# Kernel tuning notes

Hardware: AMD Instinct MI355X
Metric: run time of the kernel (lower is better)

Reference implementation:

```python
import jax, jax.numpy as jnp
import numpy as np

# ---- module hyperparams (match init_kwargs) ----
IN_CH, OUT_CH = 32, 64
KERNEL = 9
STRIDE, PADDING = 1, 4
GRID_SIZE, SPLINE_ORDER = 5, 3
GRID_LO, GRID_HI = -1.0, 1.0
NUM_COEF = GRID_SIZE + SPLINE_ORDER  # 8 spline basis functions


def make_grid():
    h = (GRID_HI - GRID_LO) / GRID_SIZE
    # extended knot vector, same for every input feature (efficient-KAN)
    return (jnp.arange(-SPLINE_ORDER, GRID_SIZE + SPLINE_ORDER + 1, dtype=jnp.float32) * h + GRID_LO)


def b_splines(x, grid, order):
    """Cox-de Boor B-spline bases. x: (...,) -> (..., NUM_COEF)."""
    x = x[..., None]
    bases = ((x >= grid[:-1]) & (x < grid[1:])).astype(x.dtype)
    for k in range(1, order + 1):
        left = (x - grid[: -(k + 1)]) / (grid[k:-1] - grid[: -(k + 1)])
        right = (grid[k + 1:] - x) / (grid[k + 1:] - grid[1:-k])
        bases = left * bases[..., :-1] + right * bases[..., 1:]
    return bases


def setup_inputs() -> dict:
    key = jax.random.key(0)
    k1, k2, k3, k4 = jax.random.split(key, 4)
    x = jax.random.normal(k1, (16, IN_CH, 2048), dtype=jnp.float32)
    # all O*I KANLinear(kernel->1) modules batched into single tensors
    base_w = jax.random.normal(k2, (OUT_CH, IN_CH, KERNEL), dtype=jnp.float32) * (1.0 / np.sqrt(KERNEL))
    spline_w = jax.random.normal(k3, (OUT_CH, IN_CH, KERNEL, NUM_COEF), dtype=jnp.float32) * 0.1
    spline_scaler = jax.random.normal(k4, (OUT_CH, IN_CH, KERNEL), dtype=jnp.float32) * (1.0 / np.sqrt(KERNEL))
    return {"x": x, "base_w": base_w, "spline_w": spline_w, "spline_scaler": spline_scaler}


def reference(x, base_w, spline_w, spline_scaler):
    grid = make_grid()
    B, I, L = x.shape
    L_out = (L + 2 * PADDING - (KERNEL - 1) - 1) // STRIDE + 1  # dilation=1
    xp = jnp.pad(x, ((0, 0), (0, 0), (PADDING, PADDING)))
    # sliding windows: (B, I, L_out, K)
    idx = jnp.arange(L_out)[:, None] * STRIDE + jnp.arange(KERNEL)[None, :]
    win = xp[:, :, idx]
    # base branch: silu(window) . base_weight, summed over in_channels
    out = jnp.einsum('bilk,oik->bol', jax.nn.silu(win), base_w)
    # spline branch
    bs = b_splines(win, grid, SPLINE_ORDER)          # (B, I, L_out, K, C)
    sw = spline_w * spline_scaler[..., None]         # scaled spline weight
    out = out + jnp.einsum('bilkc,oikc->bol', bs, sw)
    return out
```

## Files before the change

kernel.cpp:

```cpp
#include <hip/hip_runtime.h>
#include <hip/hip_bf16.h>

namespace {

constexpr int KIN  = 32;
constexpr int KOUT = 64;
constexpr int KW   = 9;
constexpr int KPAD = 4;
constexpr int LIN  = 2048;
constexpr int KTOT = 2592;

typedef __bf16 bf16x8 __attribute__((ext_vector_type(8)));
typedef float  f32x4  __attribute__((ext_vector_type(4)));
typedef unsigned short u16x4 __attribute__((ext_vector_type(4)));
typedef unsigned short u16x8 __attribute__((ext_vector_type(8)));

__device__ __forceinline__ unsigned short f2bf(float x) {
    unsigned int u = __float_as_uint(x);
    u += 0x7FFFu + ((u >> 16) & 1u);
    return (unsigned short)(u >> 16);
}

__device__ __forceinline__ float bf2f(unsigned short h) {
    return __uint_as_float((unsigned int)h << 16);
}

#define MFMA16(a, b, c) __builtin_amdgcn_mfma_f32_16x16x32_bf16((a), (b), (c), 0, 0, 0)

__global__ __launch_bounds__(256) void kan_wprep(const float* __restrict__ base_w,
                                                 const float* __restrict__ spline_w,
                                                 const float* __restrict__ spline_scaler,
                                                 unsigned short* __restrict__ Wf) {
    unsigned int idx = blockIdx.x * 256 + threadIdx.x;
    unsigned int ch  = idx >> 8;
    unsigned int m   = (idx >> 6) & 3;
    unsigned int lane = idx & 63;
    unsigned int o  = m * 16 + (lane & 15);
    unsigned int kb = ch * 32 + (lane >> 4) * 8;

    u16x8 pk;
#pragma unroll
    for (int e = 0; e < 8; ++e) {
        unsigned int kappa = kb + e;
        unsigned int k  = kappa / 288;
        unsigned int r2 = kappa - k * 288;
        unsigned int i  = r2 / 9;
        unsigned int c  = r2 - i * 9;
        unsigned int t  = o * 288 + i * 9 + k;
        float val = (c == 0) ? base_w[t]
                             : spline_w[(size_t)t * 8 + (c - 1)] * spline_scaler[t];
        pk[e] = f2bf(val);
    }
    *(u16x8*)(Wf + (size_t)idx * 8) = pk;
}

constexpr int BN     = 64;
constexpr int TROW   = 72;
constexpr int F2COLS = 296;

__global__ __launch_bounds__(512, 4) void kan_fused(const float* __restrict__ x,
                                                    const unsigned short* __restrict__ Wf,
                                                    float* __restrict__ out) {
    __shared__ __align__(16) char smem[65536];
    unsigned short* f2t = (unsigned short*)smem;

    int tid  = threadIdx.x;
    int lane = tid & 63;
    int wv   = tid >> 6;
    int lo = lane & 15, hi = lane >> 4;

    int blk = blockIdx.x;
    int b   = blk >> 5;
    int l0  = (blk & 31) * BN;

    const int ch0 = 10 * wv;
    constexpr int NCHW = 10;
    int kk = ch0 / 9;
    int jb = ch0 - kk * 9;
    const unsigned short* wp = Wf + (size_t)ch0 * 2048 + (size_t)lane * 8;
    bf16x8 a0 = *(const bf16x8*)(wp);
    bf16x8 a1 = *(const bf16x8*)(wp + 512);
    bf16x8 a2 = *(const bf16x8*)(wp + 1024);
    bf16x8 a3 = *(const bf16x8*)(wp + 1536);

    float vv[5];
#pragma unroll
    for (int p = 0; p < 5; ++p) {
        int unit = p * 512 + tid;
        bool ok = unit < TROW * KIN;
        int i = unit / TROW;
        int r = unit - i * TROW;
        int gx = l0 + r - KPAD;
        vv[p] = 0.f;
        if (ok && gx >= 0 && gx < LIN) vv[p] = x[((size_t)b * KIN + i) * LIN + gx];
    }

    {
        f32x4 z = (f32x4){0.f, 0.f, 0.f, 0.f};
        for (int c = tid; c < TROW * F2COLS / 8; c += 512)
            *(f32x4*)(f2t + (size_t)c * 8) = z;
    }
    __syncthreads();

#pragma unroll
    for (int p = 0; p < 5; ++p) {
        int unit = p * 512 + tid;
        bool ok = unit < TROW * KIN;
        int i = unit / TROW;
        int r = unit - i * TROW;
        float v = vv[p];
        if (ok) {
            unsigned short* row = f2t + (size_t)r * F2COLS + i * 9;
            row[0] = f2bf(v / (1.f + __expf(-v)));
            float t5 = (v + 2.2f) * 2.5f;
            float mf = floorf(t5);
            int   m  = (int)mf;
            float u  = t5 - mf;
            float u2 = u * u, u3 = u2 * u;
            float w  = 1.f - u;
            float P0 = u3 * (1.f / 6.f);
            float P3 = w * w * w * (1.f / 6.f);
            float P1 = (1.f / 6.f) + 0.5f * u + 0.5f * u2 - 0.5f * u3;
            float P2 = (4.f / 6.f) - u2 + 0.5f * u3;
            int c0 = m - 3;
            if ((unsigned)(c0 + 0) <= 7u) row[1 + c0 + 0] = f2bf(P3);
            if ((unsigned)(c0 + 1) <= 7u) row[1 + c0 + 1] = f2bf(P2);
            if ((unsigned)(c0 + 2) <= 7u) row[1 + c0 + 2] = f2bf(P1);
            if ((unsigned)(c0 + 3) <= 7u) row[1 + c0 + 3] = f2bf(P0);
        }
    }
    __syncthreads();

    f32x4 acc[4][4];
#pragma unroll
    for (int m = 0; m < 4; ++m)
#pragma unroll
        for (int n = 0; n < 4; ++n) acc[m][n] = (f32x4){0.f, 0.f, 0.f, 0.f};

    const unsigned short* fp = f2t + (size_t)(lo + kk) * F2COLS + jb * 32 + hi * 8;
    bf16x8 b0 = *(const bf16x8*)(fp);
    bf16x8 b1 = *(const bf16x8*)(fp + 16 * F2COLS);
    bf16x8 b2 = *(const bf16x8*)(fp + 32 * F2COLS);
    bf16x8 b3 = *(const bf16x8*)(fp + 48 * F2COLS);

    for (int t = 0; t < NCHW; ++t) {
        bool last = (t + 1 == NCHW);
        const unsigned short* wpn = last ? wp : wp + 2048;
        int jb2 = last ? jb : jb + 1;
        const unsigned short* fpn = last ? fp : fp + ((jb2 == 9) ? (F2COLS - 8 * 32) : 32);
        if (jb2 == 9) jb2 = 0;

        bf16x8 na0 = *(const bf16x8*)(wpn);
        bf16x8 na1 = *(const bf16x8*)(wpn + 512);
        bf16x8 na2 = *(const bf16x8*)(wpn + 1024);
        bf16x8 na3 = *(const bf16x8*)(wpn + 1536);

        __builtin_amdgcn_s_setprio(1);
        acc[0][0] = MFMA16(a0, b0, acc[0][0]);
        acc[1][0] = MFMA16(a1, b0, acc[1][0]);
        acc[2][0] = MFMA16(a2, b0, acc[2][0]);
        acc[3][0] = MFMA16(a3, b0, acc[3][0]);
        b0 = *(const bf16x8*)(fpn);
        acc[0][1] = MFMA16(a0, b1, acc[0][1]);
        acc[1][1] = MFMA16(a1, b1, acc[1][1]);
        acc[2][1] = MFMA16(a2, b1, acc[2][1]);
        acc[3][1] = MFMA16(a3, b1, acc[3][1]);
        b1 = *(const bf16x8*)(fpn + 16 * F2COLS);
        acc[0][2] = MFMA16(a0, b2, acc[0][2]);
        acc[1][2] = MFMA16(a1, b2, acc[1][2]);
        acc[2][2] = MFMA16(a2, b2, acc[2][2]);
        acc[3][2] = MFMA16(a3, b2, acc[3][2]);
        b2 = *(const bf16x8*)(fpn + 32 * F2COLS);
        acc[0][3] = MFMA16(a0, b3, acc[0][3]);
        acc[1][3] = MFMA16(a1, b3, acc[1][3]);
        acc[2][3] = MFMA16(a2, b3, acc[2][3]);
        acc[3][3] = MFMA16(a3, b3, acc[3][3]);
        b3 = *(const bf16x8*)(fpn + 48 * F2COLS);
        __builtin_amdgcn_s_setprio(0);

        a0 = na0; a1 = na1; a2 = na2; a3 = na3;
        wp = wpn; fp = fpn; jb = jb2;
    }

    {
        int mq = wv & 3;
        int np = wv >> 2;
        bf16x8 a80 = *(const bf16x8*)(Wf + (size_t)80 * 2048 + (size_t)mq * 512 + (size_t)lane * 8);
        const unsigned short* fp80 = f2t + (size_t)(lo + 8) * F2COLS + 8 * 32 + hi * 8;
        bf16x8 bA = *(const bf16x8*)(fp80 + (size_t)(2 * np) * 16 * F2COLS);
        bf16x8 bB = *(const bf16x8*)(fp80 + (size_t)(2 * np + 1) * 16 * F2COLS);
        switch (wv) {
        case 0: acc[0][0] = MFMA16(a80, bA, acc[0][0]); acc[0][1] = MFMA16(a80, bB, acc[0][1]); break;
        case 1: acc[1][0] = MFMA16(a80, bA, acc[1][0]); acc[1][1] = MFMA16(a80, bB, acc[1][1]); break;
        case 2: acc[2][0] = MFMA16(a80, bA, acc[2][0]); acc[2][1] = MFMA16(a80, bB, acc[2][1]); break;
        case 3: acc[3][0] = MFMA16(a80, bA, acc[3][0]); acc[3][1] = MFMA16(a80, bB, acc[3][1]); break;
        case 4: acc[0][2] = MFMA16(a80, bA, acc[0][2]); acc[0][3] = MFMA16(a80, bB, acc[0][3]); break;
        case 5: acc[1][2] = MFMA16(a80, bA, acc[1][2]); acc[1][3] = MFMA16(a80, bB, acc[1][3]); break;
        case 6: acc[2][2] = MFMA16(a80, bA, acc[2][2]); acc[2][3] = MFMA16(a80, bB, acc[2][3]); break;
        case 7: acc[3][2] = MFMA16(a80, bA, acc[3][2]); acc[3][3] = MFMA16(a80, bB, acc[3][3]); break;
        }
    }

    __syncthreads();
    unsigned short* red16 = (unsigned short*)smem;
#pragma unroll
    for (int m = 0; m < 4; ++m)
#pragma unroll
        for (int n = 0; n < 4; ++n) {
            int sid = m * 4 + n;
            f32x4 a = acc[m][n];
            u16x4 pk = (u16x4){f2bf(a[0]), f2bf(a[1]), f2bf(a[2]), f2bf(a[3])};
            *(u16x4*)(red16 + (((size_t)sid * 8 + wv) * 64 + lane) * 4) = pk;
        }
    __syncthreads();
#pragma unroll
    for (int s = 0; s < 2; ++s) {
        int sid = wv * 2 + s;
        int m = sid >> 2, n = sid & 3;
        f32x4 acc_s = (f32x4){0.f, 0.f, 0.f, 0.f};
#pragma unroll
        for (int w = 0; w < 8; ++w) {
            u16x4 pk = *(const u16x4*)(red16 + (((size_t)sid * 8 + w) * 64 + lane) * 4);
            acc_s[0] += bf2f(pk[0]);
            acc_s[1] += bf2f(pk[1]);
            acc_s[2] += bf2f(pk[2]);
            acc_s[3] += bf2f(pk[3]);
        }
        int o = m * 16 + hi * 4;
        float* op = out + ((size_t)b * KOUT + o) * LIN + l0 + n * 16 + lo;
        op[0]               = acc_s[0];
        op[LIN]             = acc_s[1];
        op[2 * LIN]         = acc_s[2];
        op[3 * (size_t)LIN] = acc_s[3];
    }
}

}

extern "C" void kernel_launch(void* const* d_in, const int* in_sizes, int n_in,
                              void* d_out, int out_size, void* d_ws, size_t ws_size,
                              hipStream_t stream) {
    const float* x             = (const float*)d_in[0];
    const float* base_w        = (const float*)d_in[1];
    const float* spline_w      = (const float*)d_in[2];
    const float* spline_scaler = (const float*)d_in[3];
    float* out = (float*)d_out;

    unsigned short* Wf = (unsigned short*)d_ws;

    kan_wprep<<<81, 256, 0, stream>>>(base_w, spline_w, spline_scaler, Wf);
    kan_fused<<<512, 512, 0, stream>>>(x, Wf, out);
}
```

Measured before the change: 22.86 us.

## Halve block to 4 waves with 20 K-chunks each and shrink shared memory

The fused kernel now launches 256 threads (4 waves) per block instead of 512, and each wave covers 20 K-chunks instead of 10. The tail chunk and the split-K reduction are reworked for four partial sums instead of eight. Shared memory is cut from 64KB to the exact feature tile size, so more blocks can sit on a CU. This trades less cross-wave reduction traffic and better occupancy per block for a longer serial MFMA chain per wave and more loads per thread during feature generation.

```diff
diff --git a/kernel.cpp b/kernel.cpp
--- a/kernel.cpp
+++ b/kernel.cpp
@@ -58,10 +58,10 @@
 constexpr int TROW   = 72;
 constexpr int F2COLS = 296;
 
-__global__ __launch_bounds__(512, 4) void kan_fused(const float* __restrict__ x,
+__global__ __launch_bounds__(256, 3) void kan_fused(const float* __restrict__ x,
                                                     const unsigned short* __restrict__ Wf,
                                                     float* __restrict__ out) {
-    __shared__ __align__(16) char smem[65536];
+    __shared__ __align__(16) char smem[TROW * F2COLS * 2];
     unsigned short* f2t = (unsigned short*)smem;
 
     int tid  = threadIdx.x;
@@ -73,8 +73,8 @@
     int b   = blk >> 5;
     int l0  = (blk & 31) * BN;
 
-    const int ch0 = 10 * wv;
-    constexpr int NCHW = 10;
+    const int ch0 = 20 * wv;
+    constexpr int NCHW = 20;
     int kk = ch0 / 9;
     int jb = ch0 - kk * 9;
     const unsigned short* wp = Wf + (size_t)ch0 * 2048 + (size_t)lane * 8;
@@ -83,51 +83,47 @@
     bf16x8 a2 = *(const bf16x8*)(wp + 1024);
     bf16x8 a3 = *(const bf16x8*)(wp + 1536);
 
-    float vv[5];
-#pragma unroll
-    for (int p = 0; p < 5; ++p) {
-        int unit = p * 512 + tid;
-        bool ok = unit < TROW * KIN;
+    float vv[9];
+#pragma unroll
+    for (int p = 0; p < 9; ++p) {
+        int unit = p * 256 + tid;
         int i = unit / TROW;
         int r = unit - i * TROW;
         int gx = l0 + r - KPAD;
         vv[p] = 0.f;
-        if (ok && gx >= 0 && gx < LIN) vv[p] = x[((size_t)b * KIN + i) * LIN + gx];
+        if (gx >= 0 && gx < LIN) vv[p] = x[((size_t)b * KIN + i) * LIN + gx];
     }
 
     {
         f32x4 z = (f32x4){0.f, 0.f, 0.f, 0.f};
-        for (int c = tid; c < TROW * F2COLS / 8; c += 512)
+        for (int c = tid; c < TROW * F2COLS / 8; c += 256)
             *(f32x4*)(f2t + (size_t)c * 8) = z;
     }
     __syncthreads();
 
 #pragma unroll
-    for (int p = 0; p < 5; ++p) {
-        int unit = p * 512 + tid;
-        bool ok = unit < TROW * KIN;
+    for (int p = 0; p < 9; ++p) {
+        int unit = p * 256 + tid;
         int i = unit / TROW;
         int r = unit - i * TROW;
         float v = vv[p];
-        if (ok) {
-            unsigned short* row = f2t + (size_t)r * F2COLS + i * 9;
-            row[0] = f2bf(v / (1.f + __expf(-v)));
-            float t5 = (v + 2.2f) * 2.5f;
-            float mf = floorf(t5);
-            int   m  = (int)mf;
-            float u  = t5 - mf;
-            float u2 = u * u, u3 = u2 * u;
-            float w  = 1.f - u;
-            float P0 = u3 * (1.f / 6.f);
-            float P3 = w * w * w * (1.f / 6.f);
-            float P1 = (1.f / 6.f) + 0.5f * u + 0.5f * u2 - 0.5f * u3;
-            float P2 = (4.f / 6.f) - u2 + 0.5f * u3;
-            int c0 = m - 3;
-            if ((unsigned)(c0 + 0) <= 7u) row[1 + c0 + 0] = f2bf(P3);
-            if ((unsigned)(c0 + 1) <= 7u) row[1 + c0 + 1] = f2bf(P2);
-            if ((unsigned)(c0 + 2) <= 7u) row[1 + c0 + 2] = f2bf(P1);
-            if ((unsigned)(c0 + 3) <= 7u) row[1 + c0 + 3] = f2bf(P0);
-        }
+        unsigned short* row = f2t + (size_t)r * F2COLS + i * 9;
+        row[0] = f2bf(v / (1.f + __expf(-v)));
+        float t5 = (v + 2.2f) * 2.5f;
+        float mf = floorf(t5);
+        int   m  = (int)mf;
+        float u  = t5 - mf;
+        float u2 = u * u, u3 = u2 * u;
+        float w  = 1.f - u;
+        float P0 = u3 * (1.f / 6.f);
+        float P3 = w * w * w * (1.f / 6.f);
+        float P1 = (1.f / 6.f) + 0.5f * u + 0.5f * u2 - 0.5f * u3;
+        float P2 = (4.f / 6.f) - u2 + 0.5f * u3;
+        int c0 = m - 3;
+        if ((unsigned)(c0 + 0) <= 7u) row[1 + c0 + 0] = f2bf(P3);
+        if ((unsigned)(c0 + 1) <= 7u) row[1 + c0 + 1] = f2bf(P2);
+        if ((unsigned)(c0 + 2) <= 7u) row[1 + c0 + 2] = f2bf(P1);
+        if ((unsigned)(c0 + 3) <= 7u) row[1 + c0 + 3] = f2bf(P0);
     }
     __syncthreads();
 
@@ -183,21 +179,21 @@
     }
 
     {
-        int mq = wv & 3;
-        int np = wv >> 2;
-        bf16x8 a80 = *(const bf16x8*)(Wf + (size_t)80 * 2048 + (size_t)mq * 512 + (size_t)lane * 8);
+        bf16x8 a80 = *(const bf16x8*)(Wf + (size_t)80 * 2048 + (size_t)wv * 512 + (size_t)lane * 8);
         const unsigned short* fp80 = f2t + (size_t)(lo + 8) * F2COLS + 8 * 32 + hi * 8;
-        bf16x8 bA = *(const bf16x8*)(fp80 + (size_t)(2 * np) * 16 * F2COLS);
-        bf16x8 bB = *(const bf16x8*)(fp80 + (size_t)(2 * np + 1) * 16 * F2COLS);
+        bf16x8 bA = *(const bf16x8*)(fp80);
+        bf16x8 bB = *(const bf16x8*)(fp80 + 16 * F2COLS);
+        bf16x8 bC = *(const bf16x8*)(fp80 + 32 * F2COLS);
+        bf16x8 bD = *(const bf16x8*)(fp80 + 48 * F2COLS);
         switch (wv) {
-        case 0: acc[0][0] = MFMA16(a80, bA, acc[0][0]); acc[0][1] = MFMA16(a80, bB, acc[0][1]); break;
-        case 1: acc[1][0] = MFMA16(a80, bA, acc[1][0]); acc[1][1] = MFMA16(a80, bB, acc[1][1]); break;
-        case 2: acc[2][0] = MFMA16(a80, bA, acc[2][0]); acc[2][1] = MFMA16(a80, bB, acc[2][1]); break;
-        case 3: acc[3][0] = MFMA16(a80, bA, acc[3][0]); acc[3][1] = MFMA16(a80, bB, acc[3][1]); break;
-        case 4: acc[0][2] = MFMA16(a80, bA, acc[0][2]); acc[0][3] = MFMA16(a80, bB, acc[0][3]); break;
-        case 5: acc[1][2] = MFMA16(a80, bA, acc[1][2]); acc[1][3] = MFMA16(a80, bB, acc[1][3]); break;
-        case 6: acc[2][2] = MFMA16(a80, bA, acc[2][2]); acc[2][3] = MFMA16(a80, bB, acc[2][3]); break;
-        case 7: acc[3][2] = MFMA16(a80, bA, acc[3][2]); acc[3][3] = MFMA16(a80, bB, acc[3][3]); break;
+        case 0: acc[0][0]=MFMA16(a80,bA,acc[0][0]); acc[0][1]=MFMA16(a80,bB,acc[0][1]);
+                acc[0][2]=MFMA16(a80,bC,acc[0][2]); acc[0][3]=MFMA16(a80,bD,acc[0][3]); break;
+        case 1: acc[1][0]=MFMA16(a80,bA,acc[1][0]); acc[1][1]=MFMA16(a80,bB,acc[1][1]);
+                acc[1][2]=MFMA16(a80,bC,acc[1][2]); acc[1][3]=MFMA16(a80,bD,acc[1][3]); break;
+        case 2: acc[2][0]=MFMA16(a80,bA,acc[2][0]); acc[2][1]=MFMA16(a80,bB,acc[2][1]);
+                acc[2][2]=MFMA16(a80,bC,acc[2][2]); acc[2][3]=MFMA16(a80,bD,acc[2][3]); break;
+        case 3: acc[3][0]=MFMA16(a80,bA,acc[3][0]); acc[3][1]=MFMA16(a80,bB,acc[3][1]);
+                acc[3][2]=MFMA16(a80,bC,acc[3][2]); acc[3][3]=MFMA16(a80,bD,acc[3][3]); break;
         }
     }
 
@@ -210,17 +206,17 @@
             int sid = m * 4 + n;
             f32x4 a = acc[m][n];
             u16x4 pk = (u16x4){f2bf(a[0]), f2bf(a[1]), f2bf(a[2]), f2bf(a[3])};
-            *(u16x4*)(red16 + (((size_t)sid * 8 + wv) * 64 + lane) * 4) = pk;
+            *(u16x4*)(red16 + (((size_t)sid * 4 + wv) * 64 + lane) * 4) = pk;
         }
     __syncthreads();
 #pragma unroll
-    for (int s = 0; s < 2; ++s) {
-        int sid = wv * 2 + s;
+    for (int s = 0; s < 4; ++s) {
+        int sid = wv * 4 + s;
         int m = sid >> 2, n = sid & 3;
         f32x4 acc_s = (f32x4){0.f, 0.f, 0.f, 0.f};
 #pragma unroll
-        for (int w = 0; w < 8; ++w) {
-            u16x4 pk = *(const u16x4*)(red16 + (((size_t)sid * 8 + w) * 64 + lane) * 4);
+        for (int w = 0; w < 4; ++w) {
+            u16x4 pk = *(const u16x4*)(red16 + (((size_t)sid * 4 + w) * 64 + lane) * 4);
             acc_s[0] += bf2f(pk[0]);
             acc_s[1] += bf2f(pk[1]);
             acc_s[2] += bf2f(pk[2]);
@@ -249,5 +245,5 @@
     unsigned short* Wf = (unsigned short*)d_ws;
 
     kan_wprep<<<81, 256, 0, stream>>>(base_w, spline_w, spline_scaler, Wf);
-    kan_fused<<<512, 512, 0, stream>>>(x, Wf, out);
-}
+    kan_fused<<<512, 256, 0, stream>>>(x, Wf, out);
+}
```

New measurement: 23.11 us. No clear change (+1.1%).
